# Optimization experiments

Hardware: AMD Instinct MI355X
Metric: run time of the kernel (lower is better)

The kernel has to match this reference:

```python
import jax, jax.numpy as jnp
import numpy as np


def setup_inputs() -> dict:
    key = jax.random.key(0)
    k1, k2, k3, k4 = jax.random.split(key, 4)
    B, T, F_in, F_out, N, E, K = 16, 64, 64, 64, 128, 2, 4
    x = jax.random.normal(k1, (B, T, F_in, N), dtype=jnp.float32)
    # graph shift operator per (batch, time, edge-feature); scaled to keep powers bounded
    S = jax.random.normal(k2, (B, T, E, N, N), dtype=jnp.float32) / np.sqrt(N)
    H = jax.random.normal(k3, (F_out, E, K, F_in), dtype=jnp.float32) * 0.02
    bias = jax.random.normal(k4, (F_out, 1), dtype=jnp.float32) * 0.02
    return {"x": x, "S": S, "H": H, "bias": bias}


def reference(x, S, H, bias):
    # x: [B,T,F_in,N], S: [B,T,E,N,N], H: [F_out,E,K,F_in], bias: [F_out,1]
    B, T, F_in, N = x.shape
    E = S.shape[2]
    F_out, _, K, _ = H.shape
    # replicate features across edge-feature dim: [B,T,E,F_in,N]
    cur = jnp.broadcast_to(x[:, :, None], (B, T, E, F_in, N))
    taps = [cur]
    zero_row = jnp.zeros((B, 1, E, F_in, N), dtype=x.dtype)
    for _ in range(1, K):
        # time-shift: tap k at time t depends on tap k-1 at time t-1
        cur = jnp.concatenate([zero_row, cur[:, :-1]], axis=1)
        # diffuse over graph: [..,F_in,N] @ [..,N,N]
        cur = jnp.matmul(cur, S)
        taps.append(cur)
    z = jnp.stack(taps, axis=2)  # [B,T,K,E,F_in,N]
    # [B,T,N, E*K*F_in], matching permute(0,1,5,3,2,4) in the source
    z = z.transpose(0, 1, 5, 3, 2, 4).reshape(B, T, N, E * K * F_in)
    Hm = H.reshape(F_out, E * K * F_in)
    y = jnp.einsum('btnf,of->bton', z, Hm)  # [B,T,F_out,N]
    return y + bias  # bias [F_out,1] broadcasts over N
```

## Files before the change

kernel.cpp:

```cpp
#include <hip/hip_runtime.h>


namespace {
constexpr int B = 16, T = 64, F = 64, N = 128, E = 2, K = 4;
constexpr int SH = 72;
constexpr int SX = 72;
constexpr int SA = 136;
}

typedef short v8s __attribute__((ext_vector_type(8)));
typedef float v4f __attribute__((ext_vector_type(4)));

__device__ inline ushort f2bf(float f) {
  union { float f; uint u; } v; v.f = f;
  uint u = v.u;
  return (ushort)((u + 0x7fffu + ((u >> 16) & 1u)) >> 16);
}

__device__ inline uint4 pack8(const ushort* p) {
  uint4 w;
  w.x = (uint)p[0] | ((uint)p[1] << 16);
  w.y = (uint)p[2] | ((uint)p[3] << 16);
  w.z = (uint)p[4] | ((uint)p[5] << 16);
  w.w = (uint)p[6] | ((uint)p[7] << 16);
  return w;
}

__global__ __launch_bounds__(256) void cvt_H(const float* __restrict__ H,
                                             ushort* __restrict__ Hb) {
  const int d4 = blockIdx.x * 256 + threadIdx.x;
  const int d = d4 * 4;
  const int f = d & 63, o = (d >> 6) & 63, k = (d >> 12) & 3, e = (d >> 14) & 1;
  const float4 v = *(const float4*)(H + (((size_t)o * E + e) * K + k) * F + f);
  uint2 w;
  w.x = (uint)f2bf(v.x) | ((uint)f2bf(v.y) << 16);
  w.y = (uint)f2bf(v.z) | ((uint)f2bf(v.w) << 16);
  *(uint2*)(Hb + d) = w;
}

__global__ __launch_bounds__(256) void cvt_S(const float* __restrict__ S,
                                             ushort* __restrict__ ST) {
  __shared__ ushort tile[128 * 130];
  const int bid = blockIdx.x;
  const float* Sg = S + (size_t)bid * N * N;
  ushort* Og = ST + (size_t)bid * N * N;
  const int tid = threadIdx.x;
  #pragma unroll
  for (int it = 0; it < 16; ++it) {
    const int idx = tid + it * 256;
    const int m = idx >> 5, n4 = (idx & 31) * 4;
    const float4 v = *(const float4*)(Sg + m * N + n4);
    uint* lp = (uint*)&tile[m * 130 + n4];
    lp[0] = (uint)f2bf(v.x) | ((uint)f2bf(v.y) << 16);
    lp[1] = (uint)f2bf(v.z) | ((uint)f2bf(v.w) << 16);
  }
  __syncthreads();
  #pragma unroll
  for (int it = 0; it < 4; ++it) {
    const int idx = tid + it * 256;
    const int m8 = (idx & 15) * 8, n2 = idx >> 4;
    uint r[8];
    #pragma unroll
    for (int j = 0; j < 8; ++j)
      r[j] = *(const uint*)&tile[(m8 + j) * 130 + 2 * n2];
    uint4 w0, w1;
    w0.x = (r[0] & 0xffffu) | (r[1] << 16);
    w0.y = (r[2] & 0xffffu) | (r[3] << 16);
    w0.z = (r[4] & 0xffffu) | (r[5] << 16);
    w0.w = (r[6] & 0xffffu) | (r[7] << 16);
    w1.x = (r[0] >> 16) | (r[1] & 0xffff0000u);
    w1.y = (r[2] >> 16) | (r[3] & 0xffff0000u);
    w1.z = (r[4] >> 16) | (r[5] & 0xffff0000u);
    w1.w = (r[6] >> 16) | (r[7] & 0xffff0000u);
    *(uint4*)(Og + (2 * n2) * N + m8) = w0;
    *(uint4*)(Og + (2 * n2 + 1) * N + m8) = w1;
  }
}

__device__ inline void stage_Hb(const ushort* __restrict__ Hb, int e, int k,
                                ushort* sH, int tid) {
  const ushort* src = Hb + (size_t)((e * K + k) * 64) * 64;
  #pragma unroll
  for (int it = 0; it < 2; ++it) {
    const int idx = tid + it * 256;
    const int o = idx >> 3, f8 = (idx & 7) * 8;
    *(uint4*)&sH[o * SH + f8] = *(const uint4*)(src + o * 64 + f8);
  }
}

__device__ inline void stage_X(const float* __restrict__ xg, ushort* sB, int tid) {
  #pragma unroll
  for (int it = 0; it < 4; ++it) {
    const int idx = tid + it * 256;
    const int n = idx & 127, f8 = (idx >> 7) * 8;
    ushort p[8];
    #pragma unroll
    for (int j = 0; j < 8; ++j) p[j] = f2bf(xg[(f8 + j) * N + n]);
    *(uint4*)&sB[n * SX + f8] = pack8(p);
  }
}

__device__ inline void stage_Sh(const ushort* __restrict__ STg, int h,
                                ushort* sB, int tid) {
  #pragma unroll
  for (int it = 0; it < 4; ++it) {
    const int idx = tid + it * 256;
    const int n = idx >> 3, m8 = (idx & 7) * 8;
    *(uint4*)&sB[n * SX + m8] = *(const uint4*)(STg + n * N + h * 64 + m8);
  }
}

__device__ inline void zero_acc(v4f acc[2][4]) {
  #pragma unroll
  for (int i = 0; i < 2; ++i)
    #pragma unroll
    for (int j = 0; j < 4; ++j) {
      acc[i][j][0] = 0.f; acc[i][j][1] = 0.f; acc[i][j][2] = 0.f; acc[i][j][3] = 0.f;
    }
}

__device__ inline void do_proj(const ushort* sH, const ushort* sB, v4f acc[2][4],
                               int ob0, int nb0, int l15, int q) {
  #pragma unroll
  for (int fk = 0; fk < 2; ++fk) {
    v8s a[2], bb[4];
    #pragma unroll
    for (int mt = 0; mt < 2; ++mt)
      a[mt] = *(const v8s*)&sH[(ob0 + 16 * mt + l15) * SH + fk * 32 + q * 8];
    #pragma unroll
    for (int nt = 0; nt < 4; ++nt)
      bb[nt] = *(const v8s*)&sB[(nb0 + 16 * nt + l15) * SX + fk * 32 + q * 8];
    #pragma unroll
    for (int mt = 0; mt < 2; ++mt)
      #pragma unroll
      for (int nt = 0; nt < 4; ++nt)
        acc[mt][nt] = __builtin_amdgcn_mfma_f32_16x16x32_bf16(
            a[mt], bb[nt], acc[mt][nt], 0, 0, 0);
  }
}

__device__ inline void do_mm(const ushort* sA, const ushort* sB, int h,
                             v4f acc[2][4], int ob0, int nb0, int l15, int q) {
  #pragma unroll
  for (int lk = 0; lk < 2; ++lk) {
    v8s a[2], bb[4];
    #pragma unroll
    for (int mt = 0; mt < 2; ++mt)
      a[mt] = *(const v8s*)&sA[(ob0 + 16 * mt + l15) * SA + h * 64 + lk * 32 + q * 8];
    #pragma unroll
    for (int nt = 0; nt < 4; ++nt)
      bb[nt] = *(const v8s*)&sB[(nb0 + 16 * nt + l15) * SX + lk * 32 + q * 8];
    #pragma unroll
    for (int mt = 0; mt < 2; ++mt)
      #pragma unroll
      for (int nt = 0; nt < 4; ++nt)
        acc[mt][nt] = __builtin_amdgcn_mfma_f32_16x16x32_bf16(
            a[mt], bb[nt], acc[mt][nt], 0, 0, 0);
  }
}

__device__ inline void store_sA(ushort* sA, v4f acc[2][4],
                                int ob0, int nb0, int l15, int q) {
  #pragma unroll
  for (int mt = 0; mt < 2; ++mt)
    #pragma unroll
    for (int nt = 0; nt < 4; ++nt) {
      const int col = nb0 + 16 * nt + l15;
      #pragma unroll
      for (int r = 0; r < 4; ++r)
        sA[(ob0 + 16 * mt + q * 4 + r) * SA + col] = f2bf(acc[mt][nt][r]);
    }
}

__global__ __launch_bounds__(256, 3) void gf_fused(
    const float* __restrict__ x, const ushort* __restrict__ ST,
    const ushort* __restrict__ Hb, const float* __restrict__ bias,
    float* __restrict__ y) {
  __shared__ ushort sH[64 * SH];
  __shared__ ushort sB[128 * SX];
  __shared__ ushort sA[64 * SA];
  const int bid = blockIdx.x;
  const int t = bid % T, b = bid / T;
  const int tid = threadIdx.x, w = tid >> 6, lane = tid & 63;
  const int l15 = lane & 15, q = lane >> 4;
  const int ob0 = (w & 1) * 32, nb0 = (w >> 1) * 64;

  v4f accY[2][4];
  v4f acc[2][4];
  zero_acc(accY);

  for (int e = 0; e < E; ++e) {
    bool have = false;
    zero_acc(acc);
    #pragma unroll
    for (int k = 3; k >= 0; --k) {
      const int s = t - k;
      if (s < 0) continue;
      const bool prevP = have;
      __syncthreads();
      if (prevP) store_sA(sA, acc, ob0, nb0, l15, q);
      stage_Hb(Hb, e, k, sH, tid);
      stage_X(x + (size_t)(b * T + s) * F * N, sB, tid);
      __syncthreads();
      if (k == 0) {
        do_proj(sH, sB, accY, ob0, nb0, l15, q);
      } else {
        zero_acc(acc);
        do_proj(sH, sB, acc, ob0, nb0, l15, q);
      }
      if (prevP) {
        const ushort* STg = ST + (size_t)((b * T + s) * E + e) * N * N;
        #pragma unroll
        for (int h = 0; h < 2; ++h) {
          __syncthreads();
          stage_Sh(STg, h, sB, tid);
          __syncthreads();
          if (k == 0) do_mm(sA, sB, h, accY, ob0, nb0, l15, q);
          else        do_mm(sA, sB, h, acc,  ob0, nb0, l15, q);
        }
      }
      have = true;
    }
  }

  float* yg = y + (size_t)(b * T + t) * F * N;
  #pragma unroll
  for (int mt = 0; mt < 2; ++mt)
    #pragma unroll
    for (int nt = 0; nt < 4; ++nt) {
      const int col = nb0 + 16 * nt + l15;
      #pragma unroll
      for (int r = 0; r < 4; ++r) {
        const int row = ob0 + 16 * mt + q * 4 + r;
        yg[row * N + col] = accY[mt][nt][r] + bias[row];
      }
    }
}

extern "C" void kernel_launch(void* const* d_in, const int* in_sizes, int n_in,
                              void* d_out, int out_size, void* d_ws, size_t ws_size,
                              hipStream_t stream) {
  const float* x    = (const float*)d_in[0];
  const float* S    = (const float*)d_in[1];
  const float* H    = (const float*)d_in[2];
  const float* bias = (const float*)d_in[3];
  float* y = (float*)d_out;

  const size_t STn = (size_t)B * T * E * N * N;
  ushort* ST = (ushort*)d_ws;
  ushort* Hb = ST + STn;

  cvt_H   <<<32,        256, 0, stream>>>(H, Hb);
  cvt_S   <<<B * T * E, 256, 0, stream>>>(S, ST);
  gf_fused<<<B * T,     256, 0, stream>>>(x, ST, Hb, bias, y);
}
```

Before: 332.0 us.

## Split fused graph filter into Horner-style per-tap kernels sharing intermediate results

Replaces the per-output-time recomputation of all K taps with a Horner-style recurrence across separate launches: project with H_k, add the previous time's partial result times S, and repeat down to tap 0. Intermediates are written to workspace in bf16. x is pre-transposed to bf16 once, and the S conversion now writes a plain transposed layout. This removes redundant diffusion matmuls (each S is now used about once per tap level instead of many times) and the in-kernel x conversion, at the cost of extra launches, global round trips for intermediates, and extra bf16 rounding of partial sums.

```diff
diff --git a/kernel.cpp b/kernel.cpp
--- a/kernel.cpp
+++ b/kernel.cpp
@@ -3,9 +3,7 @@
 
 namespace {
 constexpr int B = 16, T = 64, F = 64, N = 128, E = 2, K = 4;
-constexpr int SH = 72;
-constexpr int SX = 72;
-constexpr int SA = 136;
+constexpr int SS = 136;
 }
 
 typedef short v8s __attribute__((ext_vector_type(8)));
@@ -15,15 +13,6 @@
   union { float f; uint u; } v; v.f = f;
   uint u = v.u;
   return (ushort)((u + 0x7fffu + ((u >> 16) & 1u)) >> 16);
-}
-
-__device__ inline uint4 pack8(const ushort* p) {
-  uint4 w;
-  w.x = (uint)p[0] | ((uint)p[1] << 16);
-  w.y = (uint)p[2] | ((uint)p[3] << 16);
-  w.z = (uint)p[4] | ((uint)p[5] << 16);
-  w.w = (uint)p[6] | ((uint)p[7] << 16);
-  return w;
 }
 
 __global__ __launch_bounds__(256) void cvt_H(const float* __restrict__ H,
@@ -38,6 +27,39 @@
   *(uint2*)(Hb + d) = w;
 }
 
+__global__ __launch_bounds__(256) void cvt_X(const float* __restrict__ x,
+                                             ushort* __restrict__ xT) {
+  __shared__ ushort tile[64 * 130];
+  const int bid = blockIdx.x;
+  const float* xg = x + (size_t)bid * F * N;
+  ushort* Og = xT + (size_t)bid * N * F;
+  const int tid = threadIdx.x;
+  #pragma unroll
+  for (int it = 0; it < 8; ++it) {
+    const int idx = tid + it * 256;
+    const int f = idx >> 5, n4 = (idx & 31) * 4;
+    const float4 v = *(const float4*)(xg + f * N + n4);
+    uint* lp = (uint*)&tile[f * 130 + n4];
+    lp[0] = (uint)f2bf(v.x) | ((uint)f2bf(v.y) << 16);
+    lp[1] = (uint)f2bf(v.z) | ((uint)f2bf(v.w) << 16);
+  }
+  __syncthreads();
+  #pragma unroll
+  for (int it = 0; it < 4; ++it) {
+    const int idx = tid + it * 256;
+    const int n = idx >> 3, f8 = (idx & 7) * 8;
+    ushort p[8];
+    #pragma unroll
+    for (int j = 0; j < 8; ++j) p[j] = tile[(f8 + j) * 130 + n];
+    uint4 w;
+    w.x = (uint)p[0] | ((uint)p[1] << 16);
+    w.y = (uint)p[2] | ((uint)p[3] << 16);
+    w.z = (uint)p[4] | ((uint)p[5] << 16);
+    w.w = (uint)p[6] | ((uint)p[7] << 16);
+    *(uint4*)(Og + n * F + f8) = w;
+  }
+}
+
 __global__ __launch_bounds__(256) void cvt_S(const float* __restrict__ S,
                                              ushort* __restrict__ ST) {
   __shared__ ushort tile[128 * 130];
@@ -56,57 +78,58 @@
   }
   __syncthreads();
   #pragma unroll
-  for (int it = 0; it < 4; ++it) {
-    const int idx = tid + it * 256;
-    const int m8 = (idx & 15) * 8, n2 = idx >> 4;
-    uint r[8];
-    #pragma unroll
-    for (int j = 0; j < 8; ++j)
-      r[j] = *(const uint*)&tile[(m8 + j) * 130 + 2 * n2];
-    uint4 w0, w1;
-    w0.x = (r[0] & 0xffffu) | (r[1] << 16);
-    w0.y = (r[2] & 0xffffu) | (r[3] << 16);
-    w0.z = (r[4] & 0xffffu) | (r[5] << 16);
-    w0.w = (r[6] & 0xffffu) | (r[7] << 16);
-    w1.x = (r[0] >> 16) | (r[1] & 0xffff0000u);
-    w1.y = (r[2] >> 16) | (r[3] & 0xffff0000u);
-    w1.z = (r[4] >> 16) | (r[5] & 0xffff0000u);
-    w1.w = (r[6] >> 16) | (r[7] & 0xffff0000u);
-    *(uint4*)(Og + (2 * n2) * N + m8) = w0;
-    *(uint4*)(Og + (2 * n2 + 1) * N + m8) = w1;
-  }
-}
-
-__device__ inline void stage_Hb(const ushort* __restrict__ Hb, int e, int k,
-                                ushort* sH, int tid) {
-  const ushort* src = Hb + (size_t)((e * K + k) * 64) * 64;
-  #pragma unroll
-  for (int it = 0; it < 2; ++it) {
-    const int idx = tid + it * 256;
-    const int o = idx >> 3, f8 = (idx & 7) * 8;
-    *(uint4*)&sH[o * SH + f8] = *(const uint4*)(src + o * 64 + f8);
-  }
-}
-
-__device__ inline void stage_X(const float* __restrict__ xg, ushort* sB, int tid) {
-  #pragma unroll
-  for (int it = 0; it < 4; ++it) {
-    const int idx = tid + it * 256;
-    const int n = idx & 127, f8 = (idx >> 7) * 8;
+  for (int it = 0; it < 8; ++it) {
+    const int idx = tid + it * 256;
+    const int n = idx >> 4, m8 = (idx & 15) * 8;
     ushort p[8];
     #pragma unroll
-    for (int j = 0; j < 8; ++j) p[j] = f2bf(xg[(f8 + j) * N + n]);
-    *(uint4*)&sB[n * SX + f8] = pack8(p);
-  }
-}
-
-__device__ inline void stage_Sh(const ushort* __restrict__ STg, int h,
-                                ushort* sB, int tid) {
-  #pragma unroll
-  for (int it = 0; it < 4; ++it) {
-    const int idx = tid + it * 256;
-    const int n = idx >> 3, m8 = (idx & 7) * 8;
-    *(uint4*)&sB[n * SX + m8] = *(const uint4*)(STg + n * N + h * 64 + m8);
+    for (int j = 0; j < 8; ++j) p[j] = tile[(m8 + j) * 130 + n];
+    uint4 w;
+    w.x = (uint)p[0] | ((uint)p[1] << 16);
+    w.y = (uint)p[2] | ((uint)p[3] << 16);
+    w.z = (uint)p[4] | ((uint)p[5] << 16);
+    w.w = (uint)p[6] | ((uint)p[7] << 16);
+    *(uint4*)(Og + n * N + m8) = w;
+  }
+}
+
+__device__ inline void load_hf(const ushort* __restrict__ Hb, int e, int k,
+                               int ob0, int l15, int q, v8s hf[2][2]) {
+  #pragma unroll
+  for (int mt = 0; mt < 2; ++mt)
+    #pragma unroll
+    for (int fk = 0; fk < 2; ++fk)
+      hf[mt][fk] = *(const v8s*)(Hb +
+          ((size_t)((e * K + k) * 64 + ob0 + 16 * mt + l15)) * 64 + fk * 32 + q * 8);
+}
+
+__device__ inline void load_xf(const ushort* __restrict__ xb,
+                               int nb0, int l15, int q, v8s xf[4][2]) {
+  #pragma unroll
+  for (int nt = 0; nt < 4; ++nt)
+    #pragma unroll
+    for (int fk = 0; fk < 2; ++fk)
+      xf[nt][fk] = *(const v8s*)(xb + (nb0 + 16 * nt + l15) * F + fk * 32 + q * 8);
+}
+
+__device__ inline void load_pf(const ushort* __restrict__ Pg,
+                               int ob0, int l15, int q, v8s pf[2][2][2]) {
+  #pragma unroll
+  for (int mt = 0; mt < 2; ++mt)
+    #pragma unroll
+    for (int h = 0; h < 2; ++h)
+      #pragma unroll
+      for (int lk = 0; lk < 2; ++lk)
+        pf[mt][h][lk] = *(const v8s*)(Pg +
+            (ob0 + 16 * mt + l15) * N + h * 64 + lk * 32 + q * 8);
+}
+
+__device__ inline void stage_S(const ushort* __restrict__ STg, ushort* sS, int tid) {
+  #pragma unroll
+  for (int it = 0; it < 8; ++it) {
+    const int idx = tid + it * 256;
+    const int n = idx >> 4, m8 = (idx & 15) * 8;
+    *(uint4*)&sS[n * SS + m8] = *(const uint4*)(STg + n * N + m8);
   }
 }
 
@@ -119,48 +142,39 @@
     }
 }
 
-__device__ inline void do_proj(const ushort* sH, const ushort* sB, v4f acc[2][4],
-                               int ob0, int nb0, int l15, int q) {
-  #pragma unroll
-  for (int fk = 0; fk < 2; ++fk) {
-    v8s a[2], bb[4];
-    #pragma unroll
-    for (int mt = 0; mt < 2; ++mt)
-      a[mt] = *(const v8s*)&sH[(ob0 + 16 * mt + l15) * SH + fk * 32 + q * 8];
-    #pragma unroll
-    for (int nt = 0; nt < 4; ++nt)
-      bb[nt] = *(const v8s*)&sB[(nb0 + 16 * nt + l15) * SX + fk * 32 + q * 8];
+__device__ inline void do_proj(const v8s hf[2][2], const v8s xf[4][2],
+                               v4f acc[2][4]) {
+  #pragma unroll
+  for (int fk = 0; fk < 2; ++fk)
     #pragma unroll
     for (int mt = 0; mt < 2; ++mt)
       #pragma unroll
       for (int nt = 0; nt < 4; ++nt)
         acc[mt][nt] = __builtin_amdgcn_mfma_f32_16x16x32_bf16(
-            a[mt], bb[nt], acc[mt][nt], 0, 0, 0);
-  }
-}
-
-__device__ inline void do_mm(const ushort* sA, const ushort* sB, int h,
-                             v4f acc[2][4], int ob0, int nb0, int l15, int q) {
-  #pragma unroll
-  for (int lk = 0; lk < 2; ++lk) {
-    v8s a[2], bb[4];
-    #pragma unroll
-    for (int mt = 0; mt < 2; ++mt)
-      a[mt] = *(const v8s*)&sA[(ob0 + 16 * mt + l15) * SA + h * 64 + lk * 32 + q * 8];
-    #pragma unroll
-    for (int nt = 0; nt < 4; ++nt)
-      bb[nt] = *(const v8s*)&sB[(nb0 + 16 * nt + l15) * SX + lk * 32 + q * 8];
-    #pragma unroll
-    for (int mt = 0; mt < 2; ++mt)
+            hf[mt][fk], xf[nt][fk], acc[mt][nt], 0, 0, 0);
+}
+
+__device__ inline void do_mm(const v8s pf[2][2][2], const ushort* sS,
+                             v4f acc[2][4], int nb0, int l15, int q) {
+  #pragma unroll
+  for (int h = 0; h < 2; ++h)
+    #pragma unroll
+    for (int lk = 0; lk < 2; ++lk) {
+      v8s bb[4];
       #pragma unroll
       for (int nt = 0; nt < 4; ++nt)
-        acc[mt][nt] = __builtin_amdgcn_mfma_f32_16x16x32_bf16(
-            a[mt], bb[nt], acc[mt][nt], 0, 0, 0);
-  }
-}
-
-__device__ inline void store_sA(ushort* sA, v4f acc[2][4],
-                                int ob0, int nb0, int l15, int q) {
+        bb[nt] = *(const v8s*)&sS[(nb0 + 16 * nt + l15) * SS + h * 64 + lk * 32 + q * 8];
+      #pragma unroll
+      for (int mt = 0; mt < 2; ++mt)
+        #pragma unroll
+        for (int nt = 0; nt < 4; ++nt)
+          acc[mt][nt] = __builtin_amdgcn_mfma_f32_16x16x32_bf16(
+              pf[mt][h][lk], bb[nt], acc[mt][nt], 0, 0, 0);
+    }
+}
+
+__device__ inline void store_W(ushort* __restrict__ Og, v4f acc[2][4],
+                               int ob0, int nb0, int l15, int q) {
   #pragma unroll
   for (int mt = 0; mt < 2; ++mt)
     #pragma unroll
@@ -168,62 +182,93 @@
       const int col = nb0 + 16 * nt + l15;
       #pragma unroll
       for (int r = 0; r < 4; ++r)
-        sA[(ob0 + 16 * mt + q * 4 + r) * SA + col] = f2bf(acc[mt][nt][r]);
-    }
-}
-
-__global__ __launch_bounds__(256, 3) void gf_fused(
-    const float* __restrict__ x, const ushort* __restrict__ ST,
-    const ushort* __restrict__ Hb, const float* __restrict__ bias,
-    float* __restrict__ y) {
-  __shared__ ushort sH[64 * SH];
-  __shared__ ushort sB[128 * SX];
-  __shared__ ushort sA[64 * SA];
-  const int bid = blockIdx.x;
-  const int t = bid % T, b = bid / T;
+        Og[(ob0 + 16 * mt + q * 4 + r) * N + col] = f2bf(acc[mt][nt][r]);
+    }
+}
+
+__global__ __launch_bounds__(256, 4) void gf_proj(
+    const ushort* __restrict__ xT, const ushort* __restrict__ Hb,
+    ushort* __restrict__ Out, int k) {
+  const int bid = blockIdx.x;
+  const int e = bid & 1, bs = bid >> 1;
   const int tid = threadIdx.x, w = tid >> 6, lane = tid & 63;
   const int l15 = lane & 15, q = lane >> 4;
   const int ob0 = (w & 1) * 32, nb0 = (w >> 1) * 64;
-
-  v4f accY[2][4];
+  v8s hf[2][2], xf[4][2];
+  load_hf(Hb, e, k, ob0, l15, q, hf);
+  load_xf(xT + (size_t)bs * N * F, nb0, l15, q, xf);
   v4f acc[2][4];
-  zero_acc(accY);
-
+  zero_acc(acc);
+  do_proj(hf, xf, acc);
+  store_W(Out + (size_t)bid * F * N, acc, ob0, nb0, l15, q);
+}
+
+__global__ __launch_bounds__(256, 4) void gf_step(
+    const ushort* __restrict__ xT, const ushort* __restrict__ ST,
+    const ushort* __restrict__ Hb, const ushort* __restrict__ Pin,
+    ushort* __restrict__ Out, int k) {
+  __shared__ ushort sS[128 * SS];
+  const int bid = blockIdx.x;
+  const int e = bid & 1, bs = bid >> 1;
+  const int s = bs & (T - 1);
+  const int tid = threadIdx.x, w = tid >> 6, lane = tid & 63;
+  const int l15 = lane & 15, q = lane >> 4;
+  const int ob0 = (w & 1) * 32, nb0 = (w >> 1) * 64;
+  const bool has_p = (s > 0);
+
+  if (has_p) stage_S(ST + (size_t)bid * N * N, sS, tid);
+
+  v8s hf[2][2], xf[4][2];
+  load_hf(Hb, e, k, ob0, l15, q, hf);
+  load_xf(xT + (size_t)bs * N * F, nb0, l15, q, xf);
+
+  v4f acc[2][4];
+  zero_acc(acc);
+  do_proj(hf, xf, acc);
+
+  if (has_p) {
+    v8s pf[2][2][2];
+    load_pf(Pin + (size_t)((bs - 1) * E + e) * F * N, ob0, l15, q, pf);
+    __syncthreads();
+    do_mm(pf, sS, acc, nb0, l15, q);
+  }
+  store_W(Out + (size_t)bid * F * N, acc, ob0, nb0, l15, q);
+}
+
+__global__ __launch_bounds__(256, 4) void gf_final(
+    const ushort* __restrict__ xT, const ushort* __restrict__ ST,
+    const ushort* __restrict__ Hb, const ushort* __restrict__ Pin,
+    const float* __restrict__ bias, float* __restrict__ y) {
+  __shared__ ushort sS[128 * SS];
+  const int bid = blockIdx.x;
+  const int t = bid & (T - 1);
+  const int tid = threadIdx.x, w = tid >> 6, lane = tid & 63;
+  const int l15 = lane & 15, q = lane >> 4;
+  const int ob0 = (w & 1) * 32, nb0 = (w >> 1) * 64;
+  const bool has_p = (t > 0);
+
+  v4f acc[2][4];
+  zero_acc(acc);
+
+  #pragma unroll
   for (int e = 0; e < E; ++e) {
-    bool have = false;
-    zero_acc(acc);
-    #pragma unroll
-    for (int k = 3; k >= 0; --k) {
-      const int s = t - k;
-      if (s < 0) continue;
-      const bool prevP = have;
+    if (has_p) {
+      if (e > 0) __syncthreads();
+      stage_S(ST + (size_t)(bid * E + e) * N * N, sS, tid);
+    }
+    v8s hf[2][2], xf[4][2];
+    load_hf(Hb, e, 0, ob0, l15, q, hf);
+    load_xf(xT + (size_t)bid * N * F, nb0, l15, q, xf);
+    do_proj(hf, xf, acc);
+    if (has_p) {
+      v8s pf[2][2][2];
+      load_pf(Pin + (size_t)((bid - 1) * E + e) * F * N, ob0, l15, q, pf);
       __syncthreads();
-      if (prevP) store_sA(sA, acc, ob0, nb0, l15, q);
-      stage_Hb(Hb, e, k, sH, tid);
-      stage_X(x + (size_t)(b * T + s) * F * N, sB, tid);
-      __syncthreads();
-      if (k == 0) {
-        do_proj(sH, sB, accY, ob0, nb0, l15, q);
-      } else {
-        zero_acc(acc);
-        do_proj(sH, sB, acc, ob0, nb0, l15, q);
-      }
-      if (prevP) {
-        const ushort* STg = ST + (size_t)((b * T + s) * E + e) * N * N;
-        #pragma unroll
-        for (int h = 0; h < 2; ++h) {
-          __syncthreads();
-          stage_Sh(STg, h, sB, tid);
-          __syncthreads();
-          if (k == 0) do_mm(sA, sB, h, accY, ob0, nb0, l15, q);
-          else        do_mm(sA, sB, h, acc,  ob0, nb0, l15, q);
-        }
-      }
-      have = true;
-    }
-  }
-
-  float* yg = y + (size_t)(b * T + t) * F * N;
+      do_mm(pf, sS, acc, nb0, l15, q);
+    }
+  }
+
+  float* yg = y + (size_t)bid * F * N;
   #pragma unroll
   for (int mt = 0; mt < 2; ++mt)
     #pragma unroll
@@ -232,7 +277,7 @@
       #pragma unroll
       for (int r = 0; r < 4; ++r) {
         const int row = ob0 + 16 * mt + q * 4 + r;
-        yg[row * N + col] = accY[mt][nt][r] + bias[row];
+        yg[row * N + col] = acc[mt][nt][r] + bias[row];
       }
     }
 }
@@ -247,10 +292,19 @@
   float* y = (float*)d_out;
 
   const size_t STn = (size_t)B * T * E * N * N;
+  const size_t XTn = (size_t)B * T * N * F;
+  const size_t Wn  = (size_t)B * T * E * F * N;
   ushort* ST = (ushort*)d_ws;
-  ushort* Hb = ST + STn;
+  ushort* xT = ST + STn;
+  ushort* Wa = xT + XTn;
+  ushort* Wb = Wa + Wn;
+  ushort* Hb = Wb + Wn;
 
   cvt_H   <<<32,        256, 0, stream>>>(H, Hb);
+  cvt_X   <<<B * T,     256, 0, stream>>>(x, xT);
   cvt_S   <<<B * T * E, 256, 0, stream>>>(S, ST);
-  gf_fused<<<B * T,     256, 0, stream>>>(x, ST, Hb, bias, y);
-}
+  gf_proj <<<B * T * E, 256, 0, stream>>>(xT, Hb, Wa, 3);
+  gf_step <<<B * T * E, 256, 0, stream>>>(xT, ST, Hb, Wa, Wb, 2);
+  gf_step <<<B * T * E, 256, 0, stream>>>(xT, ST, Hb, Wb, Wa, 1);
+  gf_final<<<B * T,     256, 0, stream>>>(xT, ST, Hb, Wa, bias, y);
+}
```

New measurement: 343.3 us. +3.4%, slower.
